# Performance work log

Measured on AMD Instinct MI355X. Metric: run time of the kernel, lower is better.

Reference implementation:

```python
import jax, jax.numpy as jnp
import numpy as np

NUM_USERS = 100000
NUM_BOOKS = 50000
N_NODES = NUM_USERS + NUM_BOOKS
LATENT = 64
NUM_LAYERS = 3
N_EDGES = 2400000


def setup_inputs() -> dict:
    key = jax.random.key(0)
    ks = jax.random.split(key, 12)
    edge_index = jax.random.randint(ks[0], (2, N_EDGES), 0, N_NODES)
    embedding = jax.random.normal(ks[1], (N_NODES, LATENT), dtype=jnp.float32) * 0.1
    user_features = jax.random.normal(ks[2], (NUM_USERS, 16), dtype=jnp.float32)
    book_numerical_features = jax.random.normal(ks[3], (NUM_BOOKS, 8), dtype=jnp.float32)
    book_genre_features = jax.random.normal(ks[4], (NUM_BOOKS, 32), dtype=jnp.float32)
    W_user = jax.random.normal(ks[5], (16, LATENT), dtype=jnp.float32) * 0.1
    b_user = jnp.zeros((LATENT,), dtype=jnp.float32)
    W_num = jax.random.normal(ks[6], (8, LATENT), dtype=jnp.float32) * 0.1
    b_num = jnp.zeros((LATENT,), dtype=jnp.float32)
    W_genre = jax.random.normal(ks[7], (32, LATENT), dtype=jnp.float32) * 0.1
    b_genre = jnp.zeros((LATENT,), dtype=jnp.float32)
    return {
        "edge_index": edge_index,
        "embedding": embedding,
        "user_features": user_features,
        "book_numerical_features": book_numerical_features,
        "book_genre_features": book_genre_features,
        "W_user": W_user, "b_user": b_user,
        "W_num": W_num, "b_num": b_num,
        "W_genre": W_genre, "b_genre": b_genre,
    }


def reference(edge_index, embedding, user_features, book_numerical_features,
              book_genre_features, W_user, b_user, W_num, b_num, W_genre, b_genre):
    N = embedding.shape[0]
    # feature projections fused into initial embedding (emb0)
    user_proj = user_features @ W_user + b_user                       # [Nu, D]
    book_proj = (book_numerical_features @ W_num + b_num
                 + book_genre_features @ W_genre + b_genre)           # [Nb, D]
    emb0 = embedding + jnp.concatenate([user_proj, book_proj], axis=0)  # [N, D]

    frm, to = edge_index[0], edge_index[1]
    # symmetric degree normalization: deg counts incoming edges at target nodes
    deg = jax.ops.segment_sum(jnp.ones_like(to, dtype=emb0.dtype), to, num_segments=N)
    deg_inv_sqrt = jnp.where(deg > 0, deg ** -0.5, 0.0)
    norm = deg_inv_sqrt[frm] * deg_inv_sqrt[to]                       # [E]

    # LightGCN: gather -> scale -> scatter-add, then mean over all layer outputs
    emb = emb0
    acc = emb0
    for _ in range(NUM_LAYERS):
        msg = norm[:, None] * emb[frm]                                # [E, D]
        emb = jax.ops.segment_sum(msg, to, num_segments=N)            # [N, D]
        acc = acc + emb
    out = acc / (NUM_LAYERS + 1)
    return emb0, out
```

## Files before the change

### kernel.cpp

```cpp
#include <hip/hip_runtime.h>
#include <hip/hip_bf16.h>

typedef __hip_bfloat16 bf16;

#define D 64
#define BSH 8
#define CAP 5120
#define EPB 16384
#define PTB 1024
#define NPW 8
#define GNP 4


__global__ __launch_bounds__(1024) void k_part(const int* __restrict__ frm,
                                               const int* __restrict__ to,
                                               int* __restrict__ gcur,
                                               int* __restrict__ be, int E, int nbk) {
    __shared__ int hist[1024];
    __shared__ int lofs[1024];
    __shared__ int gbase[1024];
    __shared__ int wsum[16];
    __shared__ int stage[EPB];

    int tid = threadIdx.x;
    hist[tid] = 0;
    __syncthreads();

    int base = blockIdx.x * EPB;
    int  f[16], bk[16], tl[16];
    bool va[16];
    #pragma unroll
    for (int k = 0; k < 16; k++) {
        int i = base + k * PTB + tid;
        va[k] = (i < E);
        int ic = va[k] ? i : base;
        int t = to[ic];
        f[k]  = frm[ic];
        bk[k] = t >> BSH;
        tl[k] = t & 255;
        if (va[k]) atomicAdd(&hist[bk[k]], 1);
    }
    __syncthreads();

    int c = hist[tid];
    int lane = tid & 63, wv = tid >> 6;
    int x = c;
    #pragma unroll
    for (int off = 1; off < 64; off <<= 1) {
        int y = __shfl_up(x, off);
        if (lane >= off) x += y;
    }
    if (lane == 63) wsum[wv] = x;
    __syncthreads();
    if (wv == 0) {
        int wval = (lane < 16) ? wsum[lane] : 0;
        #pragma unroll
        for (int off = 1; off < 16; off <<= 1) {
            int y = __shfl_up(wval, off);
            if (lane >= off) wval += y;
        }
        if (lane < 16) wsum[lane] = wval;
    }
    __syncthreads();
    int excl = x + (wv ? wsum[wv - 1] : 0) - c;
    lofs[tid]  = excl;
    gbase[tid] = (c > 0 && tid < nbk) ? (tid * CAP + atomicAdd(&gcur[tid], c)) : 0;
    hist[tid]  = excl;
    __syncthreads();

    #pragma unroll
    for (int k = 0; k < 16; k++) {
        if (va[k]) {
            int p = atomicAdd(&hist[bk[k]], 1);
            stage[p] = (f[k] << 8) | tl[k];
        }
    }
    __syncthreads();

    for (int b = wv; b < nbk; b += 16) {
        int ls = lofs[b];
        int le = hist[b];
        int gd = gbase[b];
        for (int i = ls + lane; i < le; i += 64)
            be[gd + (i - ls)] = stage[i];
    }
}


__global__ __launch_bounds__(1024) void k_scatter(const int* __restrict__ gcur,
                                                  const int* __restrict__ be,
                                                  int* __restrict__ row_start,
                                                  float* __restrict__ dis,
                                                  int* __restrict__ csr,
                                                  int N, int E) {
    __shared__ int hist[256];
    __shared__ int scn[256];
    __shared__ int wred[16];
    __shared__ int bstart_s;
    int b = blockIdx.x;
    int t = threadIdx.x;
    int lane = t & 63, wv = t >> 6;

    int v = (t < b) ? gcur[t] : 0;
    #pragma unroll
    for (int off = 32; off >= 1; off >>= 1) v += __shfl_xor(v, off);
    if (lane == 0) wred[wv] = v;
    if (t < 256) hist[t] = 0;
    __syncthreads();
    if (t == 0) {
        int s = 0;
        #pragma unroll
        for (int w = 0; w < 16; w++) s += wred[w];
        bstart_s = s;
        if (b == 0) row_start[N] = E;
    }

    int base = b * CAP;
    int cnt  = gcur[b];
    for (int i = t; i < cnt; i += PTB)
        atomicAdd(&hist[be[base + i] & 255], 1);
    __syncthreads();

    int d = 0;
    if (t < 256) { d = hist[t]; scn[t] = d; }
    __syncthreads();
    #pragma unroll
    for (int off = 1; off < 256; off <<= 1) {
        int s2 = 0;
        if (t < 256) s2 = scn[t] + ((t >= off) ? scn[t - off] : 0);
        __syncthreads();
        if (t < 256) scn[t] = s2;
        __syncthreads();
    }
    if (t < 256) {
        int rs = bstart_s + (scn[t] - d);
        int node = (b << BSH) + t;
        if (node < N) {
            row_start[node] = rs;
            dis[node] = (d > 0) ? rsqrtf((float)d) : 0.0f;
        }
        hist[t] = rs;
    }
    __syncthreads();

    for (int i = t; i < cnt; i += PTB) {
        int rec = be[base + i];
        int pos = atomicAdd(&hist[rec & 255], 1);
        csr[pos] = rec >> 8;
    }
}


__global__ __launch_bounds__(256) void k_emb0(const float* __restrict__ emb,
                       const float* __restrict__ uf,
                       const float* __restrict__ bn,
                       const float* __restrict__ bg,
                       const float* __restrict__ Wu,
                       const float* __restrict__ bu,
                       const float* __restrict__ Wn,
                       const float* __restrict__ bnb,
                       const float* __restrict__ Wg,
                       const float* __restrict__ bgb,
                       const float* __restrict__ dis,
                       float* __restrict__ out0, bf16* __restrict__ y0,
                       int N, int NU, int ublocks) {
    int lane = threadIdx.x & 63;
    int wsub = __builtin_amdgcn_readfirstlane(threadIdx.x >> 6);

    if (blockIdx.x < ublocks) {
        float w[16];
        #pragma unroll
        for (int k = 0; k < 16; k++) w[k] = Wu[k * D + lane];
        float bias = bu[lane];

        int node0 = (blockIdx.x * 4 + wsub) * NPW;
        for (int n = 0; n < NPW; n++) {
            int node = node0 + n;
            if (node >= NU) break;
            const float4* f = (const float4*)(uf + (size_t)node * 16);
            float4 f0 = f[0], f1 = f[1], f2 = f[2], f3 = f[3];
            float p = bias
                + f0.x * w[0]  + f0.y * w[1]  + f0.z * w[2]  + f0.w * w[3]
                + f1.x * w[4]  + f1.y * w[5]  + f1.z * w[6]  + f1.w * w[7]
                + f2.x * w[8]  + f2.y * w[9]  + f2.z * w[10] + f2.w * w[11]
                + f3.x * w[12] + f3.y * w[13] + f3.z * w[14] + f3.w * w[15];
            size_t idx = (size_t)node * D + lane;
            float v = emb[idx] + p;
            out0[idx] = v;
            y0[idx]   = __float2bfloat16(dis[node] * v);
        }
    } else {
        float wn[8], wg[32];
        #pragma unroll
        for (int k = 0; k < 8; k++)  wn[k] = Wn[k * D + lane];
        #pragma unroll
        for (int k = 0; k < 32; k++) wg[k] = Wg[k * D + lane];
        float bias = bnb[lane] + bgb[lane];

        int b0 = ((blockIdx.x - ublocks) * 4 + wsub) * NPW;
        for (int n = 0; n < NPW; n++) {
            int b = b0 + n;
            int node = NU + b;
            if (node >= N) break;
            const float4* fn = (const float4*)(bn + (size_t)b * 8);
            float4 n0 = fn[0], n1 = fn[1];
            const float4* fg = (const float4*)(bg + (size_t)b * 32);
            float p = bias
                + n0.x * wn[0] + n0.y * wn[1] + n0.z * wn[2] + n0.w * wn[3]
                + n1.x * wn[4] + n1.y * wn[5] + n1.z * wn[6] + n1.w * wn[7];
            #pragma unroll
            for (int q = 0; q < 8; q++) {
                float4 g = fg[q];
                p += g.x * wg[4*q]   + g.y * wg[4*q+1]
                   + g.z * wg[4*q+2] + g.w * wg[4*q+3];
            }
            size_t idx = (size_t)node * D + lane;
            float v = emb[idx] + p;
            out0[idx] = v;
            y0[idx]   = __float2bfloat16(dis[node] * v);
        }
    }
}


static __device__ __forceinline__ unsigned int pack_bf16x2(float e, float o) {
    bf16 a = __float2bfloat16(e);
    bf16 b = __float2bfloat16(o);
    unsigned short ua = __builtin_bit_cast(unsigned short, a);
    unsigned short ub = __builtin_bit_cast(unsigned short, b);
    return (unsigned int)ua | ((unsigned int)ub << 16);
}


static __device__ __forceinline__ void gather4(
        const int* __restrict__ row_start, const int* __restrict__ csr,
        const unsigned int* __restrict__ y32, int n0, int N, int lane,
        float (&a0)[GNP], float (&a1)[GNP]) {
    int half = lane >> 5;
    int lh   = lane & 31;
    int l16  = lane & 15;

    int sv[GNP], ev[GNP];
    #pragma unroll
    for (int g = 0; g < GNP; g++) {
        int node = min(n0 + g, N - 1);
        sv[g] = row_start[node];
        ev[g] = row_start[node + 1];
        a0[g] = 0.f;
        a1[g] = 0.f;
    }

    for (int c = 0; ; c++) {
        int jv[GNP], base[GNP];
        #pragma unroll
        for (int g = 0; g < GNP; g++) {
            base[g] = sv[g] + 16 * c;
            jv[g] = csr[min(base[g] + l16, max(ev[g] - 1, 0))];
        }
        #pragma unroll
        for (int u = 0; u < 8; u++) {
            #pragma unroll
            for (int g = 0; g < GNP; g++) {
                int idx = 2 * u + half;
                int j = __shfl(jv[g], idx);
                unsigned int d = y32[((unsigned int)j << 5) + lh];
                d = (base[g] + idx < ev[g]) ? d : 0u;
                a0[g] += __uint_as_float(d << 16);
                a1[g] += __uint_as_float(d & 0xffff0000u);
            }
        }
        bool cont = false;
        #pragma unroll
        for (int g = 0; g < GNP; g++) cont = cont || (base[g] + 16 < ev[g]);
        if (!cont) break;
    }

    #pragma unroll
    for (int g = 0; g < GNP; g++) {
        a0[g] += __shfl_xor(a0[g], 32);
        a1[g] += __shfl_xor(a1[g], 32);
    }
}


__global__ __launch_bounds__(256) void k_prop(const int* __restrict__ row_start,
                       const int* __restrict__ csr,
                       const float* __restrict__ dis,
                       const bf16* __restrict__ y_in,
                       bf16* __restrict__ x_out,
                       bf16* __restrict__ y_out, int N) {
    int lane = threadIdx.x & 63;
    int n0 = (blockIdx.x * 4 + (threadIdx.x >> 6)) * GNP;
    if (n0 >= N) return;

    float a0[GNP], a1[GNP];
    gather4(row_start, csr, (const unsigned int*)y_in, n0, N, lane, a0, a1);

    int half = lane >> 5;
    int lh   = lane & 31;
    #pragma unroll
    for (int g = 0; g < GNP; g++) {
        int node = n0 + g;
        if (node >= N) break;
        float dt = dis[node];
        float x0  = dt * a0[g];
        float x1v = dt * a1[g];
        unsigned int w = (unsigned int)node * 32 + lh;
        if (half == 0) {
            ((unsigned int*)x_out)[w] = pack_bf16x2(x0, x1v);
        } else {
            ((unsigned int*)y_out)[w] = pack_bf16x2(dt * x0, dt * x1v);
        }
    }
}


__global__ __launch_bounds__(256) void k_prop_last(const int* __restrict__ row_start,
                       const int* __restrict__ csr,
                       const float* __restrict__ dis,
                       const bf16* __restrict__ y_in,
                       const float* __restrict__ out0,
                       const bf16* __restrict__ x1,
                       const bf16* __restrict__ x2,
                       float* __restrict__ out1, int N) {
    int lane = threadIdx.x & 63;
    int n0 = (blockIdx.x * 4 + (threadIdx.x >> 6)) * GNP;
    if (n0 >= N) return;

    float a0[GNP], a1[GNP];
    gather4(row_start, csr, (const unsigned int*)y_in, n0, N, lane, a0, a1);

    int half = lane >> 5;
    int lh   = lane & 31;
    #pragma unroll
    for (int g = 0; g < GNP; g++) {
        int node = n0 + g;
        if (node >= N) break;
        float dt = dis[node];
        float x3e = dt * a0[g];
        float x3o = dt * a1[g];
        if (half == 0) {
            unsigned int w = (unsigned int)node * 32 + lh;
            float2 o0 = ((const float2*)out0)[w];
            unsigned int p1 = ((const unsigned int*)x1)[w];
            unsigned int p2 = ((const unsigned int*)x2)[w];
            float e1 = __uint_as_float(p1 << 16);
            float o1 = __uint_as_float(p1 & 0xffff0000u);
            float e2 = __uint_as_float(p2 << 16);
            float o2 = __uint_as_float(p2 & 0xffff0000u);
            float2 r;
            r.x = (o0.x + e1 + e2 + x3e) * 0.25f;
            r.y = (o0.y + o1 + o2 + x3o) * 0.25f;
            ((float2*)out1)[w] = r;
        }
    }
}


extern "C" void kernel_launch(void* const* d_in, const int* in_sizes, int n_in,
                              void* d_out, int out_size, void* d_ws, size_t ws_size,
                              hipStream_t stream) {
    const int E  = in_sizes[0] / 2;
    const int N  = in_sizes[1] / D;
    const int NU = in_sizes[2] / 16;
    const int nbk = (N + 255) >> BSH;

    const int*   frm = (const int*)d_in[0];
    const int*   to  = frm + E;
    const float* emb = (const float*)d_in[1];
    const float* uf  = (const float*)d_in[2];
    const float* bn  = (const float*)d_in[3];
    const float* bg  = (const float*)d_in[4];
    const float* Wu  = (const float*)d_in[5];
    const float* bu  = (const float*)d_in[6];
    const float* Wn  = (const float*)d_in[7];
    const float* bnb = (const float*)d_in[8];
    const float* Wg  = (const float*)d_in[9];
    const float* bgb = (const float*)d_in[10];

    char* p = (char*)d_ws;
    const size_t ND = (size_t)N * D;
    bf16*  y0        = (bf16*)p;   p += ND * sizeof(bf16);
    bf16*  y1        = (bf16*)p;   p += ND * sizeof(bf16);
    bf16*  x1        = (bf16*)p;   p += ND * sizeof(bf16);
    bf16*  x2        = (bf16*)p;   p += ND * sizeof(bf16);
    float* dis       = (float*)p;  p += (size_t)N * sizeof(float);
    int*   row_start = (int*)p;    p += ((size_t)N + 16) * sizeof(int);
    int*   gcur      = (int*)p;    p += (size_t)nbk * sizeof(int);
    int*   csr       = (int*)p;    p += (size_t)E * sizeof(int);
    int*   be        = (int*)p;    p += (size_t)nbk * CAP * sizeof(int);

    const int TB = 256;
    const int gridProp = (N + 4 * GNP - 1) / (4 * GNP);
    const int gridPart = (E + EPB - 1) / EPB;

    hipMemsetAsync(gcur, 0, (size_t)nbk * sizeof(int), stream);
    k_part   <<<gridPart, PTB, 0, stream>>>(frm, to, gcur, be, E, nbk);
    k_scatter<<<nbk, PTB, 0, stream>>>(gcur, be, row_start, dis, csr, N, E);

    float* out0 = (float*)d_out;
    float* out1 = out0 + ND;

    const int NB = N - NU;
    const int uwaves  = (NU + NPW - 1) / NPW;
    const int ublocks = (uwaves + 3) / 4;
    const int bwaves  = (NB + NPW - 1) / NPW;
    const int bblocks = (bwaves + 3) / 4;
    k_emb0<<<ublocks + bblocks, TB, 0, stream>>>(emb, uf, bn, bg, Wu, bu, Wn, bnb,
                                                 Wg, bgb, dis, out0, y0, N, NU, ublocks);

    k_prop     <<<gridProp, TB, 0, stream>>>(row_start, csr, dis, y0, x1, y1, N);
    k_prop     <<<gridProp, TB, 0, stream>>>(row_start, csr, dis, y1, x2, y0, N);
    k_prop_last<<<gridProp, TB, 0, stream>>>(row_start, csr, dis, y0, out0, x1, x2, out1, N);
}
```

Measured before the change: 377.8 us.

## Sort nodes by degree within each bucket to balance gather waves

The CSR build kernel now counting-sorts the nodes of each 256-node bucket by in-degree (capped at 63) and writes a permutation. The propagation kernels read node ids through this permutation, so the four nodes handled by one wave have similar degree and fewer lanes idle in the chunked gather loop. The cost is an extra indirection load per node, scattered writes of outputs in permuted order, and a little extra shared-memory work in the scatter kernel.

New measurement: 403.6 us. 1.07x slower.

```diff
diff --git a/kernel.cpp b/kernel.cpp
--- a/kernel.cpp
+++ b/kernel.cpp
@@ -92,10 +92,13 @@
                                                   int* __restrict__ row_start,
                                                   float* __restrict__ dis,
                                                   int* __restrict__ csr,
+                                                  int* __restrict__ perm,
                                                   int N, int E) {
     __shared__ int hist[256];
     __shared__ int scn[256];
     __shared__ int wred[16];
+    __shared__ int dh2[64];
+    __shared__ int dof[64];
     __shared__ int bstart_s;
     int b = blockIdx.x;
     int t = threadIdx.x;
@@ -106,6 +109,7 @@
     for (int off = 32; off >= 1; off >>= 1) v += __shfl_xor(v, off);
     if (lane == 0) wred[wv] = v;
     if (t < 256) hist[t] = 0;
+    if (t >= 256 && t < 320) dh2[t - 256] = 0;
     __syncthreads();
     if (t == 0) {
         int s = 0;
@@ -122,7 +126,13 @@
     __syncthreads();
 
     int d = 0;
-    if (t < 256) { d = hist[t]; scn[t] = d; }
+    int node = (b << BSH) + t;
+    bool vn = (t < 256) && (node < N);
+    if (t < 256) {
+        d = hist[t];
+        scn[t] = d;
+        if (vn) atomicAdd(&dh2[min(d, 63)], 1);
+    }
     __syncthreads();
     #pragma unroll
     for (int off = 1; off < 256; off <<= 1) {
@@ -132,12 +142,26 @@
         if (t < 256) scn[t] = s2;
         __syncthreads();
     }
+    if (t < 64) {
+        int c2 = dh2[t];
+        int x2 = c2;
+        #pragma unroll
+        for (int off = 1; off < 64; off <<= 1) {
+            int y2 = __shfl_up(x2, off);
+            if (lane >= off) x2 += y2;
+        }
+        dof[t] = x2 - c2;
+        dh2[t] = 0;
+    }
+    __syncthreads();
     if (t < 256) {
         int rs = bstart_s + (scn[t] - d);
-        int node = (b << BSH) + t;
-        if (node < N) {
+        if (vn) {
             row_start[node] = rs;
             dis[node] = (d > 0) ? rsqrtf((float)d) : 0.0f;
+            int bin = min(d, 63);
+            int r = atomicAdd(&dh2[bin], 1);
+            perm[(b << BSH) + dof[bin] + r] = node;
         }
         hist[t] = rs;
     }
@@ -234,8 +258,9 @@
 
 static __device__ __forceinline__ void gather4(
         const int* __restrict__ row_start, const int* __restrict__ csr,
-        const unsigned int* __restrict__ y32, int n0, int N, int lane,
-        float (&a0)[GNP], float (&a1)[GNP]) {
+        const unsigned int* __restrict__ y32, const int* __restrict__ perm,
+        int n0, int N, int lane,
+        int (&nd)[GNP], float (&a0)[GNP], float (&a1)[GNP]) {
     int half = lane >> 5;
     int lh   = lane & 31;
     int l16  = lane & 15;
@@ -243,7 +268,8 @@
     int sv[GNP], ev[GNP];
     #pragma unroll
     for (int g = 0; g < GNP; g++) {
-        int node = min(n0 + g, N - 1);
+        int node = perm[min(n0 + g, N - 1)];
+        nd[g] = node;
         sv[g] = row_start[node];
         ev[g] = row_start[node + 1];
         a0[g] = 0.f;
@@ -288,20 +314,22 @@
                        const float* __restrict__ dis,
                        const bf16* __restrict__ y_in,
                        bf16* __restrict__ x_out,
-                       bf16* __restrict__ y_out, int N) {
+                       bf16* __restrict__ y_out,
+                       const int* __restrict__ perm, int N) {
     int lane = threadIdx.x & 63;
     int n0 = (blockIdx.x * 4 + (threadIdx.x >> 6)) * GNP;
     if (n0 >= N) return;
 
+    int nd[GNP];
     float a0[GNP], a1[GNP];
-    gather4(row_start, csr, (const unsigned int*)y_in, n0, N, lane, a0, a1);
+    gather4(row_start, csr, (const unsigned int*)y_in, perm, n0, N, lane, nd, a0, a1);
 
     int half = lane >> 5;
     int lh   = lane & 31;
     #pragma unroll
     for (int g = 0; g < GNP; g++) {
-        int node = n0 + g;
-        if (node >= N) break;
+        if (n0 + g >= N) break;
+        int node = nd[g];
         float dt = dis[node];
         float x0  = dt * a0[g];
         float x1v = dt * a1[g];
@@ -322,20 +350,22 @@
                        const float* __restrict__ out0,
                        const bf16* __restrict__ x1,
                        const bf16* __restrict__ x2,
-                       float* __restrict__ out1, int N) {
+                       float* __restrict__ out1,
+                       const int* __restrict__ perm, int N) {
     int lane = threadIdx.x & 63;
     int n0 = (blockIdx.x * 4 + (threadIdx.x >> 6)) * GNP;
     if (n0 >= N) return;
 
+    int nd[GNP];
     float a0[GNP], a1[GNP];
-    gather4(row_start, csr, (const unsigned int*)y_in, n0, N, lane, a0, a1);
+    gather4(row_start, csr, (const unsigned int*)y_in, perm, n0, N, lane, nd, a0, a1);
 
     int half = lane >> 5;
     int lh   = lane & 31;
     #pragma unroll
     for (int g = 0; g < GNP; g++) {
-        int node = n0 + g;
-        if (node >= N) break;
+        if (n0 + g >= N) break;
+        int node = nd[g];
         float dt = dis[node];
         float x3e = dt * a0[g];
         float x3o = dt * a1[g];
@@ -387,6 +417,7 @@
     float* dis       = (float*)p;  p += (size_t)N * sizeof(float);
     int*   row_start = (int*)p;    p += ((size_t)N + 16) * sizeof(int);
     int*   gcur      = (int*)p;    p += (size_t)nbk * sizeof(int);
+    int*   perm      = (int*)p;    p += (size_t)N * sizeof(int);
     int*   csr       = (int*)p;    p += (size_t)E * sizeof(int);
     int*   be        = (int*)p;    p += (size_t)nbk * CAP * sizeof(int);
 
@@ -396,7 +427,7 @@
 
     hipMemsetAsync(gcur, 0, (size_t)nbk * sizeof(int), stream);
     k_part   <<<gridPart, PTB, 0, stream>>>(frm, to, gcur, be, E, nbk);
-    k_scatter<<<nbk, PTB, 0, stream>>>(gcur, be, row_start, dis, csr, N, E);
+    k_scatter<<<nbk, PTB, 0, stream>>>(gcur, be, row_start, dis, csr, perm, N, E);
 
     float* out0 = (float*)d_out;
     float* out1 = out0 + ND;
@@ -409,7 +440,8 @@
     k_emb0<<<ublocks + bblocks, TB, 0, stream>>>(emb, uf, bn, bg, Wu, bu, Wn, bnb,
                                                  Wg, bgb, dis, out0, y0, N, NU, ublocks);
 
-    k_prop     <<<gridProp, TB, 0, stream>>>(row_start, csr, dis, y0, x1, y1, N);
-    k_prop     <<<gridProp, TB, 0, stream>>>(row_start, csr, dis, y1, x2, y0, N);
-    k_prop_last<<<gridProp, TB, 0, stream>>>(row_start, csr, dis, y0, out0, x1, x2, out1, N);
-}
+    k_prop     <<<gridProp, TB, 0, stream>>>(row_start, csr, dis, y0, x1, y1, perm, N);
+    k_prop     <<<gridProp, TB, 0, stream>>>(row_start, csr, dis, y1, x2, y0, perm, N);
+    k_prop_last<<<gridProp, TB, 0, stream>>>(row_start, csr, dis, y0, out0, x1, x2,
+                                             out1, perm, N);
+}
```
